# Performance work log

Measured on AMD Instinct MI355X. Metric: run time of the kernel, lower is better.

The kernel has to match this reference:

```python
import jax, jax.numpy as jnp
import numpy as np
from jax import lax

# Config matching init_kwargs
H, W = 64, 64
DIM = 160
HEADS = 5
KD = DIM // HEADS            # key_dim = head_dim = 32 (attn_ratio=1 -> d == key_dim)
WS = 14                       # window size -> n = 196 tokens per window
HIDDEN = int(DIM * 4.0)
EPS = 1e-5


def _make_bias_idxs(ws):
    pts = [(i, j) for i in range(ws) for j in range(ws)]
    offs, idxs = {}, []
    for p1 in pts:
        for p2 in pts:
            o = (abs(p1[0] - p2[0]), abs(p1[1] - p2[1]))
            if o not in offs:
                offs[o] = len(offs)
            idxs.append(offs[o])
    n = len(pts)
    return np.asarray(idxs, np.int32).reshape(n, n), len(offs)


def setup_inputs() -> dict:
    key = jax.random.key(0)
    ks = jax.random.split(key, 10)
    bias_idxs_np, n_off = _make_bias_idxs(WS)  # [196,196], 196 unique offsets
    s = 0.02
    return {
        "x": jax.random.normal(ks[0], (16, H * W, DIM), jnp.float32),
        "ln1_g": jnp.ones((DIM,), jnp.float32),
        "ln1_b": jnp.zeros((DIM,), jnp.float32),
        "qkv_w": jax.random.normal(ks[1], (3 * KD * HEADS, DIM), jnp.float32) * s,
        "qkv_b": jnp.zeros((3 * KD * HEADS,), jnp.float32),
        "proj_w": jax.random.normal(ks[2], (DIM, KD * HEADS), jnp.float32) * s,
        "proj_b": jnp.zeros((DIM,), jnp.float32),
        "attn_biases": jax.random.normal(ks[3], (HEADS, n_off), jnp.float32) * s,
        "conv_w": jax.random.normal(ks[4], (DIM, 1, 3, 3), jnp.float32) * s,  # depthwise OIHW
        "bn_g": jnp.ones((DIM,), jnp.float32),
        "bn_b": jnp.zeros((DIM,), jnp.float32),
        "ln2_g": jnp.ones((DIM,), jnp.float32),
        "ln2_b": jnp.zeros((DIM,), jnp.float32),
        "fc1_w": jax.random.normal(ks[5], (HIDDEN, DIM), jnp.float32) * s,
        "fc1_b": jnp.zeros((HIDDEN,), jnp.float32),
        "fc2_w": jax.random.normal(ks[6], (DIM, HIDDEN), jnp.float32) * s,
        "fc2_b": jnp.zeros((DIM,), jnp.float32),
        "bias_idxs": jnp.asarray(bias_idxs_np),
    }


def _layernorm(x, g, b):
    m = jnp.mean(x, -1, keepdims=True)
    v = jnp.mean(jnp.square(x - m), -1, keepdims=True)
    return (x - m) * lax.rsqrt(v + EPS) * g + b


def reference(x, ln1_g, ln1_b, qkv_w, qkv_b, proj_w, proj_b, attn_biases,
              conv_w, bn_g, bn_b, ln2_g, ln2_b, fc1_w, fc1_b, fc2_w, fc2_b,
              bias_idxs):
    b, l, c = x.shape
    res = x
    # ---- window partition (64 -> pad 70 -> 5x5 windows of 14x14 = 196 tokens)
    pad_b = (WS - H % WS) % WS
    pad_r = (WS - W % WS) % WS
    xg = x.reshape(b, H, W, c)
    xg = jnp.pad(xg, ((0, 0), (0, pad_b), (0, pad_r), (0, 0)))
    ph, pw = H + pad_b, W + pad_r
    nh, nw = ph // WS, pw // WS
    n = WS * WS
    xw = xg.reshape(b, nh, WS, nw, WS, c).transpose(0, 1, 3, 2, 4, 5).reshape(b * nh * nw, n, c)
    # ---- attention with gathered relative-position bias
    xn = _layernorm(xw, ln1_g, ln1_b)
    qkv = (xn @ qkv_w.T + qkv_b).reshape(xw.shape[0], n, HEADS, 3 * KD)
    q, k, v = qkv[..., :KD], qkv[..., KD:2 * KD], qkv[..., 2 * KD:]
    bias = attn_biases[:, bias_idxs]  # [HEADS, n, n]
    scores = jnp.einsum('bnhd,bmhd->bhnm', q, k) * (KD ** -0.5) + bias
    a = jax.nn.softmax(scores, axis=-1)
    out = jnp.einsum('bhnm,bmhd->bnhd', a, v).reshape(xw.shape[0], n, HEADS * KD)
    xw = out @ proj_w.T + proj_b
    # ---- window merge + unpad
    xg = xw.reshape(b, nh, nw, WS, WS, c).transpose(0, 1, 3, 2, 4, 5).reshape(b, ph, pw, c)
    xg = xg[:, :H, :W]
    x = res + xg.reshape(b, l, c)
    # ---- depthwise 3x3 conv + BN (eval: running_mean=0, running_var=1)
    xc = x.transpose(0, 2, 1).reshape(b, c, H, W)
    y = lax.conv_general_dilated(xc, conv_w, (1, 1), [(1, 1), (1, 1)],
                                 dimension_numbers=('NCHW', 'OIHW', 'NCHW'),
                                 feature_group_count=c)
    y = y * (bn_g * lax.rsqrt(jnp.float32(1.0 + EPS)))[None, :, None, None] + bn_b[None, :, None, None]
    x = y.reshape(b, c, l).transpose(0, 2, 1)
    # ---- MLP with pre-LN and exact GELU
    xn = _layernorm(x, ln2_g, ln2_b)
    h = jax.nn.gelu(xn @ fc1_w.T + fc1_b, approximate=False)
    m = h @ fc2_w.T + fc2_b
    return x + m
```

## Files before the change

kernel.cpp:

```cpp
#include <hip/hip_runtime.h>
#include <hip/hip_bf16.h>
#include <math.h>

typedef unsigned short ushort;
typedef __attribute__((ext_vector_type(4))) float f32x4;
typedef __attribute__((ext_vector_type(8))) short s16x8;
typedef __attribute__((ext_vector_type(4))) short s16x4;
typedef __attribute__((ext_vector_type(4))) ushort u16x4;

#define H_    64
#define W_    64
#define DIM   160
#define HEADS 5
#define KD    32
#define WS    14
#define NTOK  196
#define NWIN  400
#define HIDDEN 640
#define EPS   1e-5f
#define NROW  (NWIN*NTOK)
#define BATCH 16
#define L_    (H_*W_)
#define MROW  (BATCH*L_)
#define CS    0.25507875861f
#define GSTRIPS 4

#if __has_builtin(__builtin_amdgcn_exp2f)
#define EXP2(x) __builtin_amdgcn_exp2f(x)
#else
#define EXP2(x) exp2f(x)
#endif

__device__ __forceinline__ ushort f2bfbits(float f) {
    unsigned u = __float_as_uint(f);
    unsigned r = (u + 0x7fffu + ((u >> 16) & 1u)) >> 16;
    return (ushort)r;
}
__device__ __forceinline__ float bf2f(ushort u) {
    return __uint_as_float(((unsigned)u) << 16);
}

__global__ __launch_bounds__(256) void pre_kernel(
    const float* __restrict__ qkv_w, const float* __restrict__ proj_w,
    const float* __restrict__ fc1_w, const float* __restrict__ fc2_w,
    const float* __restrict__ conv_w, const float* __restrict__ bn_g,
    const float* __restrict__ abias, const int* __restrict__ bidx,
    ushort* __restrict__ wb, float* __restrict__ cwT,
    ushort* __restrict__ biasPb, int n_off)
{
    const int gid = blockIdx.x * 256 + threadIdx.x;
    if (gid < 19200) {
        float4 v = ((const float4*)qkv_w)[gid];
        u16x4 o = { f2bfbits(v.x), f2bfbits(v.y), f2bfbits(v.z), f2bfbits(v.w) };
        *(u16x4*)(wb + gid * 4) = o;
    } else if (gid < 25600) {
        const int i = gid - 19200;
        float4 v = ((const float4*)proj_w)[i];
        u16x4 o = { f2bfbits(v.x), f2bfbits(v.y), f2bfbits(v.z), f2bfbits(v.w) };
        *(u16x4*)(wb + 76800 + i * 4) = o;
    } else if (gid < 38400) {
        const int idx = gid - 25600;
        const int l = idx & 63, rest = idx >> 6;
        const int jj = rest % 5, ht = rest / 5;
        const float* src = fc1_w + (size_t)(ht * 16 + (l & 15)) * 160
                         + jj * 32 + (l >> 4) * 8;
        const float4 v0 = *(const float4*)src;
        const float4 v1 = *(const float4*)(src + 4);
        u16x4 o0 = { f2bfbits(v0.x), f2bfbits(v0.y), f2bfbits(v0.z), f2bfbits(v0.w) };
        u16x4 o1 = { f2bfbits(v1.x), f2bfbits(v1.y), f2bfbits(v1.z), f2bfbits(v1.w) };
        *(u16x4*)(wb + 102400 + idx * 8)     = o0;
        *(u16x4*)(wb + 102400 + idx * 8 + 4) = o1;
    } else if (gid < 51200) {
        const int idx = gid - 38400;
        const int l = idx & 63, f = idx >> 6;
        const int dt = f % 10, u = f / 10;
        const float* base = fc2_w + (size_t)(dt * 16 + (l & 15)) * HIDDEN
                          + u * 32 + 4 * (l >> 4);
        const float4 v0 = *(const float4*)base;
        const float4 v1 = *(const float4*)(base + 16);
        u16x4 o0 = { f2bfbits(v0.x), f2bfbits(v0.y), f2bfbits(v0.z), f2bfbits(v0.w) };
        u16x4 o1 = { f2bfbits(v1.x), f2bfbits(v1.y), f2bfbits(v1.z), f2bfbits(v1.w) };
        *(u16x4*)(wb + 204800 + idx * 8)     = o0;
        *(u16x4*)(wb + 204800 + idx * 8 + 4) = o1;
    } else if (gid < 51560) {
        const int i = gid - 51200;
        const int t = i / 40, c4 = (i % 40) * 4;
#pragma unroll
        for (int j = 0; j < 4; ++j) {
            const int c = c4 + j;
            cwT[t * DIM + c] = conv_w[c * 9 + t] * bn_g[c] * rsqrtf(1.0f + EPS);
        }
    } else if (gid < 267880) {
        const int idx = gid - 51560;
        const int ln = idx & 255, f = idx >> 8;
        const int h = f / 169, rem = f % 169;
        const int qt = rem / 13, kt = rem % 13;
        int q = qt * 16 + (ln & 15); if (q > NTOK - 1) q = NTOK - 1;
        const int k0 = kt * 16 + (ln >> 4) * 4;
        ushort o[4];
#pragma unroll
        for (int r = 0; r < 4; ++r) {
            const int k = k0 + r;
            o[r] = (k < NTOK)
                ? f2bfbits(abias[h * n_off + bidx[q * NTOK + k]] * 1.4426950408889634f)
                : f2bfbits(-1e30f);
        }
        *(u16x4*)(biasPb + (size_t)idx * 4) = *(const u16x4*)o;
    }
}

__global__ __launch_bounds__(256) void ln1_win_kernel(
    const float* __restrict__ x, const float* __restrict__ g,
    const float* __restrict__ b, ushort* __restrict__ xn)
{
    const int row = blockIdx.x * 4 + (threadIdx.x >> 6);
    const int win = row / NTOK, tok = row % NTOK;
    const int bb = win / 25, wr = (win % 25) / 5, wc = win % 5;
    const int gh = wr * WS + tok / WS, gw = wc * WS + tok % WS;
    const bool valid = (gh < H_) && (gw < W_);
    const float* xrow = x + ((size_t)bb * L_ + (size_t)gh * W_ + gw) * DIM;
    const int lane = threadIdx.x & 63;
    float v0 = 0.f, v1 = 0.f, v2 = 0.f;
    if (valid) {
        v0 = xrow[lane];
        v1 = xrow[lane + 64];
        if (lane < 32) v2 = xrow[lane + 128];
    }
    float s  = v0 + v1 + v2;
    float sq = v0 * v0 + v1 * v1 + v2 * v2;
#pragma unroll
    for (int off = 32; off; off >>= 1) { s += __shfl_xor(s, off); sq += __shfl_xor(sq, off); }
    const float mean = s * (1.0f / DIM);
    const float var  = sq * (1.0f / DIM) - mean * mean;
    const float rs   = rsqrtf(var + EPS);
    ushort* orow = xn + (size_t)row * DIM;
    orow[lane]      = f2bfbits((v0 - mean) * rs * g[lane]      + b[lane]);
    orow[lane + 64] = f2bfbits((v1 - mean) * rs * g[lane + 64] + b[lane + 64]);
    if (lane < 32) orow[lane + 128] = f2bfbits((v2 - mean) * rs * g[lane + 128] + b[lane + 128]);
}

template <int EPI>
__global__ __launch_bounds__(512) void gemm_mfma(
    const ushort* __restrict__ A, const ushort* __restrict__ Wb,
    const float* __restrict__ bias, void* __restrict__ Cv,
    const float* __restrict__ extra, int M, int N)
{
    __shared__ ushort Bs[160][164];
    const int tid = threadIdx.x;
    const int wv = tid >> 6, ln = tid & 63;
    const int g = ln >> 4, l15 = ln & 15;
    const int wvm = wv & 3, wvn = wv >> 2;
    const int n0 = blockIdx.y * 160;
    const int strip0 = blockIdx.x * GSTRIPS;

    for (int e = tid; e < 160 * 20; e += 512) {
        const int row = e / 20, part = e % 20;
        *(int4*)&Bs[row][part * 8] =
            *(const int4*)(Wb + (size_t)(n0 + row) * 160 + part * 8);
    }

    s16x8 a[2][5];
    {
        const int m0 = strip0 * 128;
#pragma unroll
        for (int mt = 0; mt < 2; ++mt) {
            int am = m0 + wvm * 32 + mt * 16 + l15; if (am >= M) am = M - 1;
            const ushort* ap = A + (size_t)am * 160 + g * 8;
#pragma unroll
            for (int s = 0; s < 5; ++s) a[mt][s] = *(const s16x8*)(ap + s * 32);
        }
    }
    __syncthreads();

    for (int s = 0; s < GSTRIPS; ++s) {
        const int m0 = (strip0 + s) * 128;
        if (m0 >= M) break;

        f32x4 acc[2][5] = {};
#pragma unroll
        for (int j = 0; j < 5; ++j) {
#pragma unroll
            for (int nt = 0; nt < 5; ++nt) {
                const s16x8 bf = *(const s16x8*)&Bs[wvn * 80 + nt * 16 + l15][j * 32 + g * 8];
                acc[0][nt] = __builtin_amdgcn_mfma_f32_16x16x32_bf16(bf, a[0][j], acc[0][nt], 0, 0, 0);
                acc[1][nt] = __builtin_amdgcn_mfma_f32_16x16x32_bf16(bf, a[1][j], acc[1][nt], 0, 0, 0);
            }
        }

        if (s + 1 < GSTRIPS) {
            const int mn = (strip0 + s + 1) * 128;
#pragma unroll
            for (int mt = 0; mt < 2; ++mt) {
                int am = mn + wvm * 32 + mt * 16 + l15; if (am >= M) am = M - 1;
                const ushort* ap = A + (size_t)am * 160 + g * 8;
#pragma unroll
                for (int jj = 0; jj < 5; ++jj) a[mt][jj] = *(const s16x8*)(ap + jj * 32);
            }
        }

#pragma unroll
        for (int mt = 0; mt < 2; ++mt) {
            const int m = m0 + wvm * 32 + mt * 16 + l15;
            if (m >= M) continue;
            if (EPI == 0) {
                ushort* orow = (ushort*)Cv + (size_t)m * N;
#pragma unroll
                for (int nt = 0; nt < 5; ++nt) {
                    const int n = n0 + wvn * 80 + nt * 16 + g * 4;
                    const float4 bn = *(const float4*)&bias[n];
                    const float sc = ((n % 96) < 32) ? CS : 1.0f;
                    u16x4 o = { f2bfbits((acc[mt][nt][0] + bn.x) * sc),
                                f2bfbits((acc[mt][nt][1] + bn.y) * sc),
                                f2bfbits((acc[mt][nt][2] + bn.z) * sc),
                                f2bfbits((acc[mt][nt][3] + bn.w) * sc) };
                    *(u16x4*)(orow + n) = o;
                }
            } else {
                const int win = m / NTOK, tok = m % NTOK;
                const int bb = win / 25, wr = (win % 25) / 5, wc = win % 5;
                const int gh = wr * WS + tok / WS, gw = wc * WS + tok % WS;
                if (gh < H_ && gw < W_) {
                    const size_t rowoff = ((size_t)bb * L_ + (size_t)gh * W_ + gw) * DIM;
                    float* orow = (float*)Cv + rowoff;
                    const float* erow = extra + rowoff;
#pragma unroll
                    for (int nt = 0; nt < 5; ++nt) {
                        const int n = n0 + wvn * 80 + nt * 16 + g * 4;
                        const float4 bn = *(const float4*)&bias[n];
                        const float4 res = *(const float4*)&erow[n];
                        float4 o4 = { res.x + acc[mt][nt][0] + bn.x,
                                      res.y + acc[mt][nt][1] + bn.y,
                                      res.z + acc[mt][nt][2] + bn.z,
                                      res.w + acc[mt][nt][3] + bn.w };
                        *(float4*)&orow[n] = o4;
                    }
                }
            }
        }
    }
}

__global__ __launch_bounds__(256, 3) void mlp_fused(
    float* xo, const ushort* __restrict__ w1p, const ushort* __restrict__ w2p,
    const float* __restrict__ fc1_b, const float* __restrict__ fc2_b,
    const float* __restrict__ lng, const float* __restrict__ lnb)
{
    __shared__ ushort W1s[10240];
    __shared__ ushort W2s[10240];
    const int tid = threadIdx.x;
    const int wv = tid >> 6, ln = tid & 63;
    const int g = ln >> 4, l15 = ln & 15;
    const int row0 = blockIdx.x * 64 + wv * 16;

    const float* xp = xo + (size_t)(row0 + l15) * DIM + g * 8;
    float4 va[10];
    float vsum = 0.f, vsq = 0.f;
#pragma unroll
    for (int s = 0; s < 5; ++s) {
        const float4 p0 = *(const float4*)(xp + s * 32);
        const float4 p1 = *(const float4*)(xp + s * 32 + 4);
        va[s * 2] = p0; va[s * 2 + 1] = p1;
        vsum += (p0.x + p0.y) + (p0.z + p0.w) + (p1.x + p1.y) + (p1.z + p1.w);
        vsq  += (p0.x*p0.x + p0.y*p0.y) + (p0.z*p0.z + p0.w*p0.w)
              + (p1.x*p1.x + p1.y*p1.y) + (p1.z*p1.z + p1.w*p1.w);
    }
    vsum += __shfl_xor(vsum, 16); vsum += __shfl_xor(vsum, 32);
    vsq  += __shfl_xor(vsq, 16);  vsq  += __shfl_xor(vsq, 32);
    const float mean = vsum * (1.0f / DIM);
    const float rs = rsqrtf(vsq * (1.0f / DIM) - mean * mean + EPS);
    s16x8 a1[5];
#pragma unroll
    for (int s = 0; s < 5; ++s) {
        const float4 g0 = *(const float4*)(lng + s * 32 + g * 8);
        const float4 g1 = *(const float4*)(lng + s * 32 + g * 8 + 4);
        const float4 bb0 = *(const float4*)(lnb + s * 32 + g * 8);
        const float4 bb1 = *(const float4*)(lnb + s * 32 + g * 8 + 4);
        const float4 p0 = va[s * 2], p1 = va[s * 2 + 1];
        ushort o[8];
        o[0] = f2bfbits((p0.x - mean) * rs * g0.x + bb0.x);
        o[1] = f2bfbits((p0.y - mean) * rs * g0.y + bb0.y);
        o[2] = f2bfbits((p0.z - mean) * rs * g0.z + bb0.z);
        o[3] = f2bfbits((p0.w - mean) * rs * g0.w + bb0.w);
        o[4] = f2bfbits((p1.x - mean) * rs * g1.x + bb1.x);
        o[5] = f2bfbits((p1.y - mean) * rs * g1.y + bb1.y);
        o[6] = f2bfbits((p1.z - mean) * rs * g1.z + bb1.z);
        o[7] = f2bfbits((p1.w - mean) * rs * g1.w + bb1.w);
        a1[s] = *(const s16x8*)o;
    }

    f32x4 oacc[10] = {};
    for (int c = 0; c < 10; ++c) {
        if (c) __syncthreads();
        const ushort* s1 = w1p + c * 10240;
        const ushort* s2 = w2p + c * 10240;
        for (int e = tid; e < 1280; e += 256) {
            *(int4*)&W1s[e * 8] = *(const int4*)(s1 + e * 8);
            *(int4*)&W2s[e * 8] = *(const int4*)(s2 + e * 8);
        }
        __syncthreads();

#pragma unroll
        for (int p = 0; p < 2; ++p) {
            f32x4 h0 = {0.f,0.f,0.f,0.f}, h1 = {0.f,0.f,0.f,0.f};
#pragma unroll
            for (int jj = 0; jj < 5; ++jj) {
                const s16x8 wfe = *(const s16x8*)&W1s[(((p * 2) * 5 + jj) * 64 + ln) * 8];
                const s16x8 wfo = *(const s16x8*)&W1s[(((p * 2 + 1) * 5 + jj) * 64 + ln) * 8];
                h0 = __builtin_amdgcn_mfma_f32_16x16x32_bf16(wfe, a1[jj], h0, 0, 0, 0);
                h1 = __builtin_amdgcn_mfma_f32_16x16x32_bf16(wfo, a1[jj], h1, 0, 0, 0);
            }
            const int hb0 = c * 64 + p * 32 + g * 4;
            const float4 hbe = *(const float4*)(fc1_b + hb0);
            const float4 hbo = *(const float4*)(fc1_b + hb0 + 16);
            const float hbev[4] = { hbe.x, hbe.y, hbe.z, hbe.w };
            const float hbov[4] = { hbo.x, hbo.y, hbo.z, hbo.w };
            ushort pk[8];
#pragma unroll
            for (int r = 0; r < 4; ++r) {
                float v = h0[r] + hbev[r];
                float t = EXP2(-2.302259756f * fmaf(0.044715f * v * v, v, v));
                pk[r] = f2bfbits(v * __builtin_amdgcn_rcpf(1.0f + t));
                v = h1[r] + hbov[r];
                t = EXP2(-2.302259756f * fmaf(0.044715f * v * v, v, v));
                pk[4 + r] = f2bfbits(v * __builtin_amdgcn_rcpf(1.0f + t));
            }
            const s16x8 P = *(const s16x8*)pk;
#pragma unroll
            for (int dt = 0; dt < 10; ++dt) {
                const s16x8 w2f = *(const s16x8*)&W2s[((p * 10 + dt) * 64 + ln) * 8];
                oacc[dt] = __builtin_amdgcn_mfma_f32_16x16x32_bf16(P, w2f, oacc[dt], 0, 0, 0);
            }
        }
    }

#pragma unroll
    for (int dt = 0; dt < 10; ++dt) {
        const float bn = fc2_b[dt * 16 + l15];
#pragma unroll
        for (int r = 0; r < 4; ++r) {
            const size_t off = (size_t)(row0 + g * 4 + r) * DIM + dt * 16 + l15;
            xo[off] += oacc[dt][r] + bn;
        }
    }
}

__global__ __launch_bounds__(256) void attn_mfma_kernel(
    const ushort* __restrict__ qkv, const ushort* __restrict__ biasPb,
    ushort* __restrict__ out)
{
    __shared__ ushort Ks[208][40];
    __shared__ ushort VT[32][228];
    const int win = blockIdx.x / HEADS;
    const int h   = blockIdx.x % HEADS;
    const int tid = threadIdx.x;
    const size_t base = (size_t)win * NTOK;
    const ushort* qbase = qkv + base * 480 + h * 96;

    for (int e = tid; e < 208 * 4; e += 256) {
        const int row = e >> 2, part = e & 3;
        const int gr = row < NTOK ? row : NTOK - 1;
        *(int4*)&Ks[row][part * 8] = *(const int4*)(qbase + (size_t)gr * 480 + 32 + part * 8);
    }
    for (int e = tid; e < NTOK * 4; e += 256) {
        const int key = e >> 2, part = e & 3;
        int4 p = *(const int4*)(qbase + (size_t)key * 480 + 64 + part * 8);
        const ushort* u = (const ushort*)&p;
#pragma unroll
        for (int j = 0; j < 8; ++j) VT[part * 8 + j][key] = u[j];
    }
    for (int e = tid; e < 28 * 32; e += 256) VT[e & 31][NTOK + (e >> 5)] = 0;
    __syncthreads();

    const int wv = tid >> 6, ln = tid & 63, g = ln >> 4, l15 = ln & 15;

    for (int qt = wv; qt < 13; qt += 4) {
        const int qr = qt * 16 + l15;
        const int qc = qr < NTOK ? qr : NTOK - 1;
        const s16x8 qf = *(const s16x8*)(qbase + (size_t)qc * 480 + g * 8);
        const ushort* bq = biasPb + ((size_t)(h * 13 + qt) * 13) * 1024;

        f32x4 S[13];
#pragma unroll
        for (int kt = 0; kt < 13; ++kt) {
            const u16x4 bv = *(const u16x4*)(bq + kt * 1024 + ln * 4);
            S[kt] = (f32x4){ bf2f(bv[0]), bf2f(bv[1]), bf2f(bv[2]), bf2f(bv[3]) };
        }
#pragma unroll
        for (int kt = 0; kt < 13; ++kt) {
            const s16x8 kf = *(const s16x8*)&Ks[kt * 16 + l15][g * 8];
            S[kt] = __builtin_amdgcn_mfma_f32_16x16x32_bf16(kf, qf, S[kt], 0, 0, 0);
        }

        float sum = 0.f;
        s16x8 Pp[7];
#pragma unroll
        for (int kt = 0; kt < 13; ++kt) {
            const float p0 = EXP2(S[kt][0]);
            const float p1 = EXP2(S[kt][1]);
            const float p2 = EXP2(S[kt][2]);
            const float p3 = EXP2(S[kt][3]);
            sum += (p0 + p1) + (p2 + p3);
            const int u = kt >> 1, hi = (kt & 1) * 4;
            Pp[u][hi + 0] = (short)f2bfbits(p0);
            Pp[u][hi + 1] = (short)f2bfbits(p1);
            Pp[u][hi + 2] = (short)f2bfbits(p2);
            Pp[u][hi + 3] = (short)f2bfbits(p3);
        }
        Pp[6][4] = 0; Pp[6][5] = 0; Pp[6][6] = 0; Pp[6][7] = 0;
        sum += __shfl_xor(sum, 16);
        sum += __shfl_xor(sum, 32);

        f32x4 o0 = {0.f,0.f,0.f,0.f}, o1 = {0.f,0.f,0.f,0.f};
#pragma unroll
        for (int u = 0; u < 7; ++u) {
            const s16x4 a0lo = *(const s16x4*)&VT[l15][u * 32 + g * 4];
            const s16x4 a0hi = *(const s16x4*)&VT[l15][u * 32 + 16 + g * 4];
            const s16x4 a1lo = *(const s16x4*)&VT[16 + l15][u * 32 + g * 4];
            const s16x4 a1hi = *(const s16x4*)&VT[16 + l15][u * 32 + 16 + g * 4];
            const s16x8 A0 = { a0lo[0], a0lo[1], a0lo[2], a0lo[3],
                               a0hi[0], a0hi[1], a0hi[2], a0hi[3] };
            const s16x8 A1 = { a1lo[0], a1lo[1], a1lo[2], a1lo[3],
                               a1hi[0], a1hi[1], a1hi[2], a1hi[3] };
            o0 = __builtin_amdgcn_mfma_f32_16x16x32_bf16(A0, Pp[u], o0, 0, 0, 0);
            o1 = __builtin_amdgcn_mfma_f32_16x16x32_bf16(A1, Pp[u], o1, 0, 0, 0);
        }
        if (qr < NTOK) {
            const float inv = __builtin_amdgcn_rcpf(sum);
            ushort* op = out + (base + qr) * DIM + h * KD;
            u16x4 w0 = { f2bfbits(o0[0] * inv), f2bfbits(o0[1] * inv),
                         f2bfbits(o0[2] * inv), f2bfbits(o0[3] * inv) };
            u16x4 w1 = { f2bfbits(o1[0] * inv), f2bfbits(o1[1] * inv),
                         f2bfbits(o1[2] * inv), f2bfbits(o1[3] * inv) };
            *(u16x4*)(op + g * 4)      = w0;
            *(u16x4*)(op + 16 + g * 4) = w1;
        }
    }
}

__global__ __launch_bounds__(256) void dwconv_bn_kernel(
    const float* __restrict__ xin, const float* __restrict__ cwT,
    const float* __restrict__ bnb, float* __restrict__ xout)
{
    const int gid = blockIdx.x * 256 + threadIdx.x;
    const int pos = gid / 40, c4 = (gid % 40) * 4;
    const int bb = pos >> 12, hw = pos & 4095;
    const int hh = hw >> 6, ww = hw & 63;
    float4 acc = *(const float4*)&bnb[c4];
#pragma unroll
    for (int kh = -1; kh <= 1; ++kh) {
        const int ih = hh + kh;
        if (ih < 0 || ih >= H_) continue;
#pragma unroll
        for (int kw = -1; kw <= 1; ++kw) {
            const int iw = ww + kw;
            if (iw < 0 || iw >= W_) continue;
            const float4 xv = *(const float4*)&xin[((size_t)(bb << 12) + (ih << 6) + iw) * DIM + c4];
            const float4 wv = *(const float4*)&cwT[((kh + 1) * 3 + (kw + 1)) * DIM + c4];
            acc.x = fmaf(xv.x, wv.x, acc.x);
            acc.y = fmaf(xv.y, wv.y, acc.y);
            acc.z = fmaf(xv.z, wv.z, acc.z);
            acc.w = fmaf(xv.w, wv.w, acc.w);
        }
    }
    *(float4*)&xout[(size_t)pos * DIM + c4] = acc;
}

extern "C" void kernel_launch(void* const* d_in, const int* in_sizes, int n_in,
                              void* d_out, int out_size, void* d_ws, size_t ws_size,
                              hipStream_t stream)
{
    const float* x      = (const float*)d_in[0];
    const float* ln1_g  = (const float*)d_in[1];
    const float* ln1_b  = (const float*)d_in[2];
    const float* qkv_w  = (const float*)d_in[3];
    const float* qkv_b  = (const float*)d_in[4];
    const float* proj_w = (const float*)d_in[5];
    const float* proj_b = (const float*)d_in[6];
    const float* abias  = (const float*)d_in[7];
    const float* conv_w = (const float*)d_in[8];
    const float* bn_g   = (const float*)d_in[9];
    const float* bn_b   = (const float*)d_in[10];
    const float* ln2_g  = (const float*)d_in[11];
    const float* ln2_b  = (const float*)d_in[12];
    const float* fc1_w  = (const float*)d_in[13];
    const float* fc1_b  = (const float*)d_in[14];
    const float* fc2_w  = (const float*)d_in[15];
    const float* fc2_b  = (const float*)d_in[16];
    const int*   bidx   = (const int*)d_in[17];
    const int    n_off  = in_sizes[7] / HEADS;

    char* ws = (char*)d_ws;
    ushort* xn     = (ushort*)(ws);
    ushort* qkv    = (ushort*)(ws + 25088000);
    ushort* ao     = (ushort*)(ws + 100352000);
    ushort* biasPb = (ushort*)(ws + 125440000);
    float*  x1     = (float*)(ws + 125440000);
    ushort* wb     = (ushort*)(ws + 167383040);
    float*  cwT    = (float*)(ws + 167997440);
    float*  x2     = (float*)d_out;

    const int mblocks = (NROW + 128 * GSTRIPS - 1) / (128 * GSTRIPS);

    pre_kernel<<<dim3(1047), dim3(256), 0, stream>>>(
        qkv_w, proj_w, fc1_w, fc2_w, conv_w, bn_g, abias, bidx, wb, cwT, biasPb, n_off);

    ln1_win_kernel<<<dim3(NROW / 4), dim3(256), 0, stream>>>(x, ln1_g, ln1_b, xn);

    gemm_mfma<0><<<dim3(mblocks, 3), dim3(512), 0, stream>>>(
        xn, wb, qkv_b, (void*)qkv, nullptr, NROW, 480);

    attn_mfma_kernel<<<dim3(NWIN * HEADS), dim3(256), 0, stream>>>(qkv, biasPb, ao);

    gemm_mfma<1><<<dim3(mblocks, 1), dim3(512), 0, stream>>>(
        ao, wb + 76800, proj_b, (void*)x1, x, NROW, 160);

    dwconv_bn_kernel<<<dim3(MROW * 40 / 256), dim3(256), 0, stream>>>(
        x1, cwT, bn_b, x2);

    mlp_fused<<<dim3(MROW / 64), dim3(256), 0, stream>>>(
        x2, wb + 102400, wb + 204800, fc1_b, fc2_b, ln2_g, ln2_b);
}
```

Before: 235.1 us.

## Fuse depthwise conv + BN into MLP kernel prologue

```diff
diff --git a/kernel.cpp b/kernel.cpp
--- a/kernel.cpp
+++ b/kernel.cpp
@@ -241,7 +241,9 @@
 }
 
 __global__ __launch_bounds__(256, 3) void mlp_fused(
-    float* xo, const ushort* __restrict__ w1p, const ushort* __restrict__ w2p,
+    float* xo, const float* __restrict__ x1, const float* __restrict__ cwT,
+    const float* __restrict__ bnb,
+    const ushort* __restrict__ w1p, const ushort* __restrict__ w2p,
     const float* __restrict__ fc1_b, const float* __restrict__ fc2_b,
     const float* __restrict__ lng, const float* __restrict__ lnb)
 {
@@ -252,18 +254,46 @@
     const int g = ln >> 4, l15 = ln & 15;
     const int row0 = blockIdx.x * 64 + wv * 16;
 
-    const float* xp = xo + (size_t)(row0 + l15) * DIM + g * 8;
+    const int bi = blockIdx.x >> 6, hh = blockIdx.x & 63;
+    const int ww = wv * 16 + l15;
+    const float* x1b = x1 + ((size_t)bi << 12) * DIM;
+    float* xrow2 = xo + (size_t)(row0 + l15) * DIM;
     float4 va[10];
     float vsum = 0.f, vsq = 0.f;
 #pragma unroll
     for (int s = 0; s < 5; ++s) {
-        const float4 p0 = *(const float4*)(xp + s * 32);
-        const float4 p1 = *(const float4*)(xp + s * 32 + 4);
-        va[s * 2] = p0; va[s * 2 + 1] = p1;
-        vsum += (p0.x + p0.y) + (p0.z + p0.w) + (p1.x + p1.y) + (p1.z + p1.w);
-        vsq  += (p0.x*p0.x + p0.y*p0.y) + (p0.z*p0.z + p0.w*p0.w)
-              + (p1.x*p1.x + p1.y*p1.y) + (p1.z*p1.z + p1.w*p1.w);
-    }
+        const int c0 = s * 32 + g * 8;
+        float4 a0 = *(const float4*)&bnb[c0];
+        float4 a1v = *(const float4*)&bnb[c0 + 4];
+#pragma unroll
+        for (int kh = -1; kh <= 1; ++kh) {
+            const int ih = hh + kh;
+            if (ih < 0 || ih >= H_) continue;
+#pragma unroll
+            for (int kw = -1; kw <= 1; ++kw) {
+                const int iw = ww + kw;
+                const bool ok = (iw >= 0) && (iw < W_);
+                const int iwc = ok ? iw : ww;
+                const float* xp_ = x1b + (size_t)((ih << 6) + iwc) * DIM + c0;
+                float4 v0 = *(const float4*)xp_;
+                float4 v1 = *(const float4*)(xp_ + 4);
+                if (!ok) { v0 = make_float4(0,0,0,0); v1 = make_float4(0,0,0,0); }
+                const float4 w0 = *(const float4*)&cwT[((kh+1)*3+(kw+1))*DIM + c0];
+                const float4 w1 = *(const float4*)&cwT[((kh+1)*3+(kw+1))*DIM + c0 + 4];
+                a0.x = fmaf(v0.x, w0.x, a0.x); a0.y = fmaf(v0.y, w0.y, a0.y);
+                a0.z = fmaf(v0.z, w0.z, a0.z); a0.w = fmaf(v0.w, w0.w, a0.w);
+                a1v.x = fmaf(v1.x, w1.x, a1v.x); a1v.y = fmaf(v1.y, w1.y, a1v.y);
+                a1v.z = fmaf(v1.z, w1.z, a1v.z); a1v.w = fmaf(v1.w, w1.w, a1v.w);
+            }
+        }
+        va[s * 2] = a0; va[s * 2 + 1] = a1v;
+        *(float4*)&xrow2[c0]     = a0;
+        *(float4*)&xrow2[c0 + 4] = a1v;
+        vsum += (a0.x + a0.y) + (a0.z + a0.w) + (a1v.x + a1v.y) + (a1v.z + a1v.w);
+        vsq  += (a0.x*a0.x + a0.y*a0.y) + (a0.z*a0.z + a0.w*a0.w)
+              + (a1v.x*a1v.x + a1v.y*a1v.y) + (a1v.z*a1v.z + a1v.w*a1v.w);
+    }
+
     vsum += __shfl_xor(vsum, 16); vsum += __shfl_xor(vsum, 32);
     vsq  += __shfl_xor(vsq, 16);  vsq  += __shfl_xor(vsq, 32);
     const float mean = vsum * (1.0f / DIM);
@@ -435,34 +465,6 @@
             *(u16x4*)(op + 16 + g * 4) = w1;
         }
     }
-}
-
-__global__ __launch_bounds__(256) void dwconv_bn_kernel(
-    const float* __restrict__ xin, const float* __restrict__ cwT,
-    const float* __restrict__ bnb, float* __restrict__ xout)
-{
-    const int gid = blockIdx.x * 256 + threadIdx.x;
-    const int pos = gid / 40, c4 = (gid % 40) * 4;
-    const int bb = pos >> 12, hw = pos & 4095;
-    const int hh = hw >> 6, ww = hw & 63;
-    float4 acc = *(const float4*)&bnb[c4];
-#pragma unroll
-    for (int kh = -1; kh <= 1; ++kh) {
-        const int ih = hh + kh;
-        if (ih < 0 || ih >= H_) continue;
-#pragma unroll
-        for (int kw = -1; kw <= 1; ++kw) {
-            const int iw = ww + kw;
-            if (iw < 0 || iw >= W_) continue;
-            const float4 xv = *(const float4*)&xin[((size_t)(bb << 12) + (ih << 6) + iw) * DIM + c4];
-            const float4 wv = *(const float4*)&cwT[((kh + 1) * 3 + (kw + 1)) * DIM + c4];
-            acc.x = fmaf(xv.x, wv.x, acc.x);
-            acc.y = fmaf(xv.y, wv.y, acc.y);
-            acc.z = fmaf(xv.z, wv.z, acc.z);
-            acc.w = fmaf(xv.w, wv.w, acc.w);
-        }
-    }
-    *(float4*)&xout[(size_t)pos * DIM + c4] = acc;
 }
 
 extern "C" void kernel_launch(void* const* d_in, const int* in_sizes, int n_in,
@@ -514,9 +516,6 @@
     gemm_mfma<1><<<dim3(mblocks, 1), dim3(512), 0, stream>>>(
         ao, wb + 76800, proj_b, (void*)x1, x, NROW, 160);
 
-    dwconv_bn_kernel<<<dim3(MROW * 40 / 256), dim3(256), 0, stream>>>(
-        x1, cwT, bn_b, x2);
-
     mlp_fused<<<dim3(MROW / 64), dim3(256), 0, stream>>>(
-        x2, wb + 102400, wb + 204800, fc1_b, fc2_b, ln2_g, ln2_b);
-}
+        x2, x1, cwT, bn_b, wb + 102400, wb + 204800, fc1_b, fc2_b, ln2_g, ln2_b);
+}
```

Result: slower. 243.3 us (+3.5%).
